# Kernel optimization log

Hardware: AMD Instinct MI355X
Metric: run time of the kernel (lower is better)

The kernel has to match this reference:

```python
import jax, jax.numpy as jnp
import numpy as np

B, L, D_IN, D_MODEL, H = 8, 1024, 256, 512, 8
D_HEAD = D_MODEL // H


def setup_inputs() -> dict:
    key = jax.random.key(0)
    ks = jax.random.split(key, 12)
    queries = jax.random.normal(ks[0], (B, L, D_IN), dtype=jnp.float32)
    keys_ = jax.random.normal(ks[1], (B, L, D_IN), dtype=jnp.float32)
    values = jax.random.normal(ks[2], (B, L, D_IN), dtype=jnp.float32)
    attention_mask = jnp.ones((B, L), dtype=jnp.int32)
    # binary symmetric-ish adjacency (sparse molecular graph style)
    adjacency_matrix = (jax.random.uniform(ks[3], (B, L, L)) < 0.05).astype(jnp.float32)
    distance_matrix = jax.random.uniform(ks[4], (B, L, L), dtype=jnp.float32) * 10.0
    s = 1.0 / np.sqrt(D_IN)
    W_q = jax.random.normal(ks[5], (D_MODEL, D_IN), dtype=jnp.float32) * s
    W_k = jax.random.normal(ks[6], (D_MODEL, D_IN), dtype=jnp.float32) * s
    W_v = jax.random.normal(ks[7], (D_MODEL, D_IN), dtype=jnp.float32) * s
    W_o = jax.random.normal(ks[8], (D_MODEL, D_MODEL), dtype=jnp.float32) / np.sqrt(D_MODEL)
    lambda_a = jax.random.normal(ks[9], (H,), dtype=jnp.float32) * 0.1
    lambda_d = jax.random.normal(ks[10], (H,), dtype=jnp.float32) * 0.1
    return {"queries": queries, "keys": keys_, "values": values,
            "attention_mask": attention_mask, "adjacency_matrix": adjacency_matrix,
            "distance_matrix": distance_matrix, "W_q": W_q, "W_k": W_k,
            "W_v": W_v, "W_o": W_o, "lambda_a": lambda_a, "lambda_d": lambda_d}


def _split_heads(x):
    # (b, l, d_model) -> (b, h, l, d_head)
    b, l, _ = x.shape
    return x.reshape(b, l, H, D_HEAD).transpose(0, 2, 1, 3)


def reference(queries, keys, values, attention_mask, adjacency_matrix,
              distance_matrix, W_q, W_k, W_v, W_o, lambda_a, lambda_d):
    Q = _split_heads(queries @ W_q.T)   # (b,h,l,d)
    K = _split_heads(keys @ W_k.T)
    V = _split_heads(values @ W_v.T)
    scores = jnp.einsum("bhqd,bhkd->bhqk", Q, K) / jnp.sqrt(jnp.asarray(D_HEAD, Q.dtype))
    # MSRSA: per-head learned scalars inject graph structure into the scores
    scores = (scores
              + lambda_a[None, :, None, None] * adjacency_matrix[:, None, :, :]
              + lambda_d[None, :, None, None] * distance_matrix[:, None, :, :])
    mask = attention_mask[:, None, None, :] > 0  # (b,1,1,l) key mask
    scores = jnp.where(mask, scores, jnp.asarray(-1e9, scores.dtype))
    attn_weight = jax.nn.softmax(scores, axis=-1)  # (b,h,l,l)
    out = jnp.einsum("bhqk,bhkd->bhqd", attn_weight, V)
    out = out.transpose(0, 2, 1, 3).reshape(queries.shape[0], queries.shape[1], D_MODEL)
    return out @ W_o.T
```

## Files before the change

### kernel.cpp

```cpp
#include <hip/hip_runtime.h>
#include <hip/hip_fp16.h>

#define BB 8
#define LL 1024
#define DIN 256
#define DM 512
#define HH 8
#define DH 64

typedef __attribute__((ext_vector_type(8))) short bf16x8;
typedef __attribute__((ext_vector_type(4))) float f32x4;

__device__ __forceinline__ unsigned short f2bf(float f) {
  union { float f; unsigned u; } c; c.f = f;
  unsigned u = c.u;
  return (unsigned short)((u + 0x7fffu + ((u >> 16) & 1u)) >> 16);
}

#if defined(__has_builtin)
#if __has_builtin(__builtin_amdgcn_cvt_pk_bf16_f32)
#define HAS_PK_BF16 1
#endif
#endif

#if defined(HAS_PK_BF16)
typedef __bf16 bf2 __attribute__((ext_vector_type(2)));
__device__ __forceinline__ unsigned pk2(float lo, float hi) {
  union { bf2 v; unsigned u; } c;
  c.v = __builtin_amdgcn_cvt_pk_bf16_f32(lo, hi);
  return c.u;
}
#else
__device__ __forceinline__ unsigned pk2(float lo, float hi) {
  return ((unsigned)f2bf(hi) << 16) | f2bf(lo);
}
#endif

__device__ __forceinline__ unsigned pk16(float a, float d) {
  unsigned v = (unsigned)__half_as_ushort(__float2half_rn(d));
  v = (v + 1u) & 0xFFFEu;
  return v | (a > 0.5f ? 1u : 0u);
}
__device__ __forceinline__ unsigned pk16x2(float a0, float d0,
                                           float a1, float d1) {
  return pk16(a0, d0) | (pk16(a1, d1) << 16);
}

__device__ __forceinline__ void async_copy16(void* lds, const void* g) {
  __builtin_amdgcn_global_load_lds(
      (const __attribute__((address_space(1))) unsigned*)g,
      (__attribute__((address_space(3))) unsigned*)lds, 16, 0, 0);
}

__global__ __launch_bounds__(256) void prep(
    const float* __restrict__ qin, const float* __restrict__ kin,
    const float* __restrict__ vin,
    const float* __restrict__ wq, const float* __restrict__ wk,
    const float* __restrict__ wv, const float* __restrict__ wo,
    const int* __restrict__ msk,
    const float* __restrict__ adj, const float* __restrict__ dis,
    unsigned short* __restrict__ xq, unsigned short* __restrict__ xk,
    unsigned short* __restrict__ xv,
    unsigned short* __restrict__ wqb, unsigned short* __restrict__ wkb,
    unsigned short* __restrict__ wvb, unsigned short* __restrict__ wob,
    float* __restrict__ mad, unsigned short* __restrict__ bp)
{
  int t = blockIdx.x * 256 + threadIdx.x;
  const int XS = 524288, WS = 32768;
  if (t < 3 * XS) {
    int seg = t >> 19, off = t & (XS - 1);
    const float* s = (seg == 0) ? qin : (seg == 1) ? kin : vin;
    unsigned short* d = (seg == 0) ? xq : (seg == 1) ? xk : xv;
    float4 f = ((const float4*)s)[off];
    uint2 o = { pk2(f.x, f.y), pk2(f.z, f.w) };
    ((uint2*)d)[off] = o;
    return;
  }
  t -= 3 * XS;
  if (t < 3 * WS) {
    int seg = t >> 15, off = t & (WS - 1);
    const float* s = (seg == 0) ? wq : (seg == 1) ? wk : wv;
    unsigned short* d = (seg == 0) ? wqb : (seg == 1) ? wkb : wvb;
    float4 f = ((const float4*)s)[off];
    uint2 o = { pk2(f.x, f.y), pk2(f.z, f.w) };
    ((uint2*)d)[off] = o;
    return;
  }
  t -= 3 * WS;
  if (t < 65536) {
    float4 f = ((const float4*)wo)[t];
    uint2 o = { pk2(f.x, f.y), pk2(f.z, f.w) };
    ((uint2*)wob)[t] = o;
    return;
  }
  t -= 65536;
  if (t < 2048) {
    int4 m = ((const int4*)msk)[t];
    float4 f = { m.x ? 0.0f : -30000.0f, m.y ? 0.0f : -30000.0f,
                 m.z ? 0.0f : -30000.0f, m.w ? 0.0f : -30000.0f };
    ((float4*)mad)[t] = f;
    return;
  }
  t -= 2048;
  if (t < 1048576) {
    float4 a0 = ((const float4*)adj)[t * 2];
    float4 a1 = ((const float4*)adj)[t * 2 + 1];
    float4 d0 = ((const float4*)dis)[t * 2];
    float4 d1 = ((const float4*)dis)[t * 2 + 1];
    uint4 o = { pk16x2(a0.x, d0.x, a0.y, d0.y),
                pk16x2(a0.z, d0.z, a0.w, d0.w),
                pk16x2(a1.x, d1.x, a1.y, d1.y),
                pk16x2(a1.z, d1.z, a1.w, d1.w) };
    ((uint4*)bp)[t] = o;
  }
}

__global__ __launch_bounds__(256) void qkv_proj(
    const unsigned short* __restrict__ xq, const unsigned short* __restrict__ xk,
    const unsigned short* __restrict__ xv,
    const unsigned short* __restrict__ wqb, const unsigned short* __restrict__ wkb,
    const unsigned short* __restrict__ wvb,
    unsigned short* __restrict__ qb, unsigned short* __restrict__ kb,
    unsigned short* __restrict__ vt)
{
  const int t = blockIdx.z;
  const unsigned short* __restrict__ X = (t == 0) ? xq : (t == 1) ? xk : xv;
  const unsigned short* __restrict__ W = (t == 0) ? wqb : (t == 1) ? wkb : wvb;
  const int m0 = blockIdx.y * 128;
  const int h  = blockIdx.x;
  __shared__ __align__(16) char arena[49152];
  const int tid = threadIdx.x;
  const int wid = tid >> 6;
  const int lane = tid & 63;
  const int lo = lane & 15;
  const int quad = lane >> 4;
  char* xpriv = arena + 32768 + wid * 4096;

  f32x4 acc[2][4];
#pragma unroll
  for (int mi = 0; mi < 2; ++mi)
#pragma unroll
    for (int ni = 0; ni < 4; ++ni) acc[mi][ni] = (f32x4)0.0f;

#pragma unroll
  for (int j = 0; j < 8; ++j) {
    int idx = j * 256 + tid, r = idx >> 5, c = idx & 31;
    async_copy16(arena + j * 4096 + wid * 1024,
                 W + (size_t)(h * 64 + r) * DIN + ((c ^ (r & 15)) * 8));
  }
#pragma unroll
  for (int j = 0; j < 2; ++j) {
    int idx = j * 64 + lane, r = idx >> 2, c = idx & 3;
    async_copy16(xpriv + j * 1024,
                 X + (size_t)(m0 + wid * 32 + r) * DIN + ((c ^ (r & 3)) * 8));
  }
  __syncthreads();

  const unsigned short* Wb = (const unsigned short*)arena;
  for (int it = 0; it < 8; ++it) {
    const int p = it & 1;
    if (it < 7) {
      const int kk = (it + 1) * 32;
#pragma unroll
      for (int j = 0; j < 2; ++j) {
        int idx = j * 64 + lane, r = idx >> 2, c = idx & 3;
        async_copy16(xpriv + (1 - p) * 2048 + j * 1024,
                     X + (size_t)(m0 + wid * 32 + r) * DIN + kk +
                         ((c ^ (r & 3)) * 8));
      }
      asm volatile("" ::: "memory");
      asm volatile("s_waitcnt vmcnt(2)" ::: "memory");
    } else {
      asm volatile("s_waitcnt vmcnt(0)" ::: "memory");
    }
    const unsigned short* Ab = (const unsigned short*)(xpriv + p * 2048);
    bf16x8 a[2], bfr[4];
#pragma unroll
    for (int mi = 0; mi < 2; ++mi) {
      int R = mi * 16 + lo;
      a[mi] = *(const bf16x8*)&Ab[R * 32 + ((quad ^ (R & 3)) * 8)];
    }
#pragma unroll
    for (int ni = 0; ni < 4; ++ni) {
      int N = ni * 16 + lo;
      bfr[ni] = *(const bf16x8*)&Wb[N * 256 + (((it * 4 + quad) ^ (N & 15)) * 8)];
    }
#pragma unroll
    for (int mi = 0; mi < 2; ++mi)
#pragma unroll
      for (int ni = 0; ni < 4; ++ni)
        acc[mi][ni] = __builtin_amdgcn_mfma_f32_16x16x32_bf16(
            a[mi], bfr[ni], acc[mi][ni], 0, 0, 0);
  }

  const int b = m0 >> 10;
  const int lbase0 = (m0 & 1023) + wid * 32;
  if (t < 2) {
    unsigned short* dstp = (t == 0) ? qb : kb;
#pragma unroll
    for (int mi = 0; mi < 2; ++mi)
#pragma unroll
      for (int ni = 0; ni < 4; ++ni) {
        int d = ni * 16 + lo;
#pragma unroll
        for (int r = 0; r < 4; ++r) {
          int lb = lbase0 + mi * 16 + quad * 4 + r;
          dstp[((size_t)(b * HH + h) * LL + lb) * DH + d] = f2bf(acc[mi][ni][r]);
        }
      }
  } else {
#pragma unroll
    for (int mi = 0; mi < 2; ++mi)
#pragma unroll
      for (int ni = 0; ni < 4; ++ni) {
        int d = ni * 16 + lo;
        int lb = lbase0 + quad * 8 + mi * 4;
        uint2 o = { pk2(acc[mi][ni][0], acc[mi][ni][1]),
                    pk2(acc[mi][ni][2], acc[mi][ni][3]) };
        *(uint2*)&vt[((size_t)(b * HH + h) * DH + d) * LL + lb] = o;
      }
  }
}

__global__ __launch_bounds__(256) void attn(
    const unsigned short* __restrict__ qb, const unsigned short* __restrict__ kb,
    const unsigned short* __restrict__ vt,
    const float* __restrict__ mad, const unsigned short* __restrict__ bp,
    const float* __restrict__ la_, const float* __restrict__ ld_,
    unsigned short* __restrict__ ao)
{
  const int bi = blockIdx.x;
  const int b  = bi & 7;
  const int hg = (bi >> 3) & 3;
  const int q0 = (bi >> 5) * 32;
  const int tid = threadIdx.x;
  const int wid = tid >> 6;
  const int lane = tid & 63;
  const int lo = lane & 15;
  const int quad = lane >> 4;
  const int h  = hg * 2 + (wid & 1);
  const int kh = wid >> 1;
  const int bh = b * HH + h;

  __shared__ __align__(16) char arena[40960];
  float* mgbuf = (float*)arena;

  const float LOG2E = 1.44269504f;
  const float la2 = la_[h] * LOG2E, ld2 = ld_[h] * LOG2E;
  const float sc2 = 0.125f * LOG2E;

  const unsigned short* qp = qb + ((size_t)bh * LL + q0) * DH;
  bf16x8 qB[2][2];
#pragma unroll
  for (int nj = 0; nj < 2; ++nj)
#pragma unroll
    for (int ki = 0; ki < 2; ++ki)
      qB[nj][ki] = *(const bf16x8*)&qp[(nj * 16 + lo) * DH + ki * 32 + quad * 8];

  const unsigned short* kp = kb + (size_t)bh * LL * DH;
  const unsigned short* vp = vt + (size_t)bh * DH * LL;
  const unsigned short* bpp = bp + ((size_t)b * LL + q0) * LL;
  const float* mp = mad + b * LL;

  f32x4 o[4][2];
  float rs[2] = {0.0f, 0.0f};
#pragma unroll
  for (int md = 0; md < 4; ++md)
#pragma unroll
    for (int nj = 0; nj < 2; ++nj) o[md][nj] = (f32x4)0.0f;

  const int kbeg = kh * (LL / 2);
  const int r8 = lane >> 3, p8 = lane & 7;
  const int br = lane >> 2;
  const int bsw = ((((lane & 3) << 1) ^ (br & 6)) << 2);

  {
    const unsigned short* kg = kp + (size_t)kbeg * DH;
#pragma unroll
    for (int j = 0; j < 4; ++j)
      async_copy16(arena + wid * 4096 + j * 1024,
                   kg + (j * 8 + r8) * 64 + ((p8 ^ r8) * 8));
    if ((wid & 1) == 0) {
      const int khs = wid >> 1;
      const unsigned short* bg = bpp + khs * (LL / 2);
#pragma unroll
      for (int j = 0; j < 2; ++j)
        async_copy16(arena + 32768 + khs * 2048 + j * 1024,
                     bg + (size_t)(j * 16 + br) * LL + bsw);
    }
  }
  __syncthreads();

  for (int jt = 0; jt < 16; ++jt) {
    const int p = jt & 1;
    const int k0 = kbeg + jt * 32;

    if (jt < 15) {
      const int kn = k0 + 32, q = 1 - p;
      const unsigned short* kg = kp + (size_t)kn * DH;
#pragma unroll
      for (int j = 0; j < 4; ++j)
        async_copy16(arena + q * 16384 + wid * 4096 + j * 1024,
                     kg + (j * 8 + r8) * 64 + ((p8 ^ r8) * 8));
      if ((wid & 1) == 0) {
        const int khs = wid >> 1;
        const unsigned short* bg = bpp + khs * (LL / 2) + (jt + 1) * 32;
#pragma unroll
        for (int j = 0; j < 2; ++j)
          async_copy16(arena + 32768 + q * 4096 + khs * 2048 + j * 1024,
                       bg + (size_t)(j * 16 + br) * LL + bsw);
      }
    }

    bf16x8 vA[4];
#pragma unroll
    for (int md = 0; md < 4; ++md)
      vA[md] = *(const bf16x8*)&vp[(md * 16 + lo) * LL + k0 + quad * 8];
    f32x4 msv[2];
#pragma unroll
    for (int mi = 0; mi < 2; ++mi)
      msv[mi] = *(const f32x4*)&mp[k0 + mi * 16 + quad * 4];

    asm volatile("" ::: "memory");

    const unsigned short* kbf = (const unsigned short*)(arena + p * 16384) + wid * 2048;
    bf16x8 kA[2][2];
#pragma unroll
    for (int mi = 0; mi < 2; ++mi)
#pragma unroll
      for (int ki = 0; ki < 2; ++ki)
        kA[mi][ki] = *(const bf16x8*)&kbf[(mi * 16 + lo) * 64 +
                                          (((ki * 4 + quad) ^ (lo & 7)) * 8)];
    f32x4 s[2][2];
#pragma unroll
    for (int mi = 0; mi < 2; ++mi)
#pragma unroll
      for (int nj = 0; nj < 2; ++nj) s[mi][nj] = (f32x4)0.0f;
#pragma unroll
    for (int ki = 0; ki < 2; ++ki)
#pragma unroll
      for (int mi = 0; mi < 2; ++mi)
#pragma unroll
        for (int nj = 0; nj < 2; ++nj)
          s[mi][nj] = __builtin_amdgcn_mfma_f32_16x16x32_bf16(
              kA[mi][ki], qB[nj][ki], s[mi][nj], 0, 0, 0);

    const unsigned short* bbf =
        (const unsigned short*)(arena + 32768 + p * 4096) + kh * 1024;
    unsigned pw[2][4];
#pragma unroll
    for (int mi = 0; mi < 2; ++mi)
#pragma unroll
      for (int nj = 0; nj < 2; ++nj) {
        uint2 w = *(const uint2*)&bbf[(nj * 16 + lo) * 32 +
                                      (((mi * 4 + quad) ^ (lo & 6)) << 2)];
        float p4[4];
#pragma unroll
        for (int r = 0; r < 4; ++r) {
          unsigned xr = (((r & 2) ? w.y : w.x) >> ((r & 1) * 16)) & 0xFFFFu;
          float dv = __half2float(__ushort_as_half(
              (unsigned short)(xr & 0xFFFEu)));
          float tb = fmaf(s[mi][nj][r], sc2, msv[mi][r]);
          tb = fmaf(dv, ld2, tb);
          tb += (xr & 1u) ? la2 : 0.0f;
          p4[r] = __builtin_amdgcn_exp2f(tb);
        }
        rs[nj] += (p4[0] + p4[1]) + (p4[2] + p4[3]);
        pw[nj][mi * 2]     = pk2(p4[0], p4[1]);
        pw[nj][mi * 2 + 1] = pk2(p4[2], p4[3]);
      }
    bf16x8 pB[2];
#pragma unroll
    for (int nj = 0; nj < 2; ++nj) {
      union { unsigned u[4]; bf16x8 v; } pc;
      pc.u[0] = pw[nj][0]; pc.u[1] = pw[nj][1];
      pc.u[2] = pw[nj][2]; pc.u[3] = pw[nj][3];
      pB[nj] = pc.v;
    }

#pragma unroll
    for (int md = 0; md < 4; ++md)
#pragma unroll
      for (int nj = 0; nj < 2; ++nj)
        o[md][nj] = __builtin_amdgcn_mfma_f32_16x16x32_bf16(
            vA[md], pB[nj], o[md][nj], 0, 0, 0);

    __syncthreads();
  }

  const int hs = wid & 1;
  if (kh == 1) {
#pragma unroll
    for (int md = 0; md < 4; ++md)
#pragma unroll
      for (int nj = 0; nj < 2; ++nj)
#pragma unroll
        for (int r = 0; r < 4; ++r)
          mgbuf[hs * 2176 + ((md * 2 + nj) * 4 + r) * 64 + lane] = o[md][nj][r];
    mgbuf[hs * 2176 + 32 * 64 + lane] = rs[0];
    mgbuf[hs * 2176 + 33 * 64 + lane] = rs[1];
  }
  __syncthreads();
  if (kh == 0) {
#pragma unroll
    for (int md = 0; md < 4; ++md)
#pragma unroll
      for (int nj = 0; nj < 2; ++nj)
#pragma unroll
        for (int r = 0; r < 4; ++r)
          o[md][nj][r] += mgbuf[hs * 2176 + ((md * 2 + nj) * 4 + r) * 64 + lane];
    rs[0] += mgbuf[hs * 2176 + 32 * 64 + lane];
    rs[1] += mgbuf[hs * 2176 + 33 * 64 + lane];
    float inv[2];
#pragma unroll
    for (int nj = 0; nj < 2; ++nj) {
      rs[nj] += __shfl_xor(rs[nj], 16);
      rs[nj] += __shfl_xor(rs[nj], 32);
      inv[nj] = __builtin_amdgcn_rcpf(rs[nj]);
    }
#pragma unroll
    for (int md = 0; md < 4; ++md)
#pragma unroll
      for (int nj = 0; nj < 2; ++nj) {
        int l = q0 + nj * 16 + lo;
        uint2 st = { pk2(o[md][nj][0] * inv[nj], o[md][nj][1] * inv[nj]),
                     pk2(o[md][nj][2] * inv[nj], o[md][nj][3] * inv[nj]) };
        *(uint2*)&ao[((size_t)b * LL + l) * DM + h * DH + md * 16 + quad * 4] = st;
      }
  }
}

__global__ __launch_bounds__(256) void oproj(
    const unsigned short* __restrict__ ao, const unsigned short* __restrict__ wob,
    float* __restrict__ out)
{
  const int m0 = blockIdx.y * 128;
  const int n0 = blockIdx.x * 64;
  __shared__ __align__(16) char arena[81920];
  const int tid = threadIdx.x;
  const int wid = tid >> 6;
  const int lane = tid & 63;
  const int lo = lane & 15;
  const int quad = lane >> 4;
  char* xpriv = arena + 65536 + wid * 4096;

  f32x4 acc[2][4];
#pragma unroll
  for (int mi = 0; mi < 2; ++mi)
#pragma unroll
    for (int ni = 0; ni < 4; ++ni) acc[mi][ni] = (f32x4)0.0f;

#pragma unroll
  for (int j = 0; j < 16; ++j) {
    int idx = j * 256 + tid, r = idx >> 6, c = idx & 63;
    async_copy16(arena + j * 4096 + wid * 1024,
                 wob + (size_t)(n0 + r) * DM + ((c ^ (r & 15)) * 8));
  }
#pragma unroll
  for (int j = 0; j < 2; ++j) {
    int idx = j * 64 + lane, r = idx >> 2, c = idx & 3;
    async_copy16(xpriv + j * 1024,
                 ao + (size_t)(m0 + wid * 32 + r) * DM + ((c ^ (r & 3)) * 8));
  }
  __syncthreads();

  const unsigned short* Wb = (const unsigned short*)arena;
  for (int it = 0; it < 16; ++it) {
    const int p = it & 1;
    if (it < 15) {
      const int kk = (it + 1) * 32;
#pragma unroll
      for (int j = 0; j < 2; ++j) {
        int idx = j * 64 + lane, r = idx >> 2, c = idx & 3;
        async_copy16(xpriv + (1 - p) * 2048 + j * 1024,
                     ao + (size_t)(m0 + wid * 32 + r) * DM + kk +
                         ((c ^ (r & 3)) * 8));
      }
      asm volatile("" ::: "memory");
      asm volatile("s_waitcnt vmcnt(2)" ::: "memory");
    } else {
      asm volatile("s_waitcnt vmcnt(0)" ::: "memory");
    }
    const unsigned short* Ab = (const unsigned short*)(xpriv + p * 2048);
    bf16x8 a[2], bfr[4];
#pragma unroll
    for (int mi = 0; mi < 2; ++mi) {
      int R = mi * 16 + lo;
      a[mi] = *(const bf16x8*)&Ab[R * 32 + ((quad ^ (R & 3)) * 8)];
    }
#pragma unroll
    for (int ni = 0; ni < 4; ++ni) {
      int N = ni * 16 + lo;
      bfr[ni] = *(const bf16x8*)&Wb[N * 512 + (((it * 4 + quad) ^ (N & 15)) * 8)];
    }
#pragma unroll
    for (int mi = 0; mi < 2; ++mi)
#pragma unroll
      for (int ni = 0; ni < 4; ++ni)
        acc[mi][ni] = __builtin_amdgcn_mfma_f32_16x16x32_bf16(
            a[mi], bfr[ni], acc[mi][ni], 0, 0, 0);
  }

#pragma unroll
  for (int mi = 0; mi < 2; ++mi)
#pragma unroll
    for (int ni = 0; ni < 4; ++ni)
#pragma unroll
      for (int r = 0; r < 4; ++r)
        out[(size_t)(m0 + wid * 32 + mi * 16 + quad * 4 + r) * DM +
            n0 + ni * 16 + lo] = acc[mi][ni][r];
}

extern "C" void kernel_launch(void* const* d_in, const int* in_sizes, int n_in,
                              void* d_out, int out_size, void* d_ws, size_t ws_size,
                              hipStream_t stream) {
  const float* qin = (const float*)d_in[0];
  const float* kin = (const float*)d_in[1];
  const float* vin = (const float*)d_in[2];
  const int*   msk = (const int*)d_in[3];
  const float* adj = (const float*)d_in[4];
  const float* dis = (const float*)d_in[5];
  const float* wq  = (const float*)d_in[6];
  const float* wk  = (const float*)d_in[7];
  const float* wv  = (const float*)d_in[8];
  const float* wo  = (const float*)d_in[9];
  const float* la  = (const float*)d_in[10];
  const float* ld  = (const float*)d_in[11];
  float* out = (float*)d_out;

  const size_t tensb = (size_t)BB * HH * LL * DH;
  const size_t xsz   = (size_t)BB * LL * DIN;
  unsigned short* qb  = (unsigned short*)d_ws;
  unsigned short* kb  = qb + tensb;
  unsigned short* vt  = kb + tensb;
  unsigned short* ao  = vt + tensb;
  unsigned short* xq  = ao;
  unsigned short* xk  = ao + xsz;
  unsigned short* xv  = ao + tensb;
  unsigned short* wqb = xv + xsz;
  unsigned short* wkb = wqb + (size_t)DM * DIN;
  unsigned short* wvb = wkb + (size_t)DM * DIN;
  unsigned short* wob = wvb + (size_t)DM * DIN;
  float*          mdd = (float*)(wob + (size_t)DM * DM);
  unsigned short* bpk = (unsigned short*)(mdd + (size_t)BB * LL);

  prep<<<dim3(10888), 256, 0, stream>>>(qin, kin, vin, wq, wk, wv, wo, msk,
                                        adj, dis,
                                        xq, xk, xv, wqb, wkb, wvb, wob, mdd, bpk);
  qkv_proj<<<dim3(8, 64, 3), 256, 0, stream>>>(xq, xk, xv, wqb, wkb, wvb, qb, kb, vt);
  attn<<<dim3(1024), 256, 0, stream>>>(qb, kb, vt, mdd, bpk, la, ld, ao);
  oproj<<<dim3(8, 64), 256, 0, stream>>>(ao, wob, out);
}
```

Baseline: 230.7 us.

## Use per-wave private LDS buffers and drop per-iteration block barriers

Each wave now owns its own K tile (single-buffered) and its own double-buffered copy of the bias tile in LDS, so the per-iteration __syncthreads is replaced by explicit vmcnt/lgkmcnt waits. The next K tile is prefetched into the same buffer right after its LDS reads complete, and the bias tile is now loaded redundantly by both head waves instead of being shared. This removes block-wide barrier stalls and cuts LDS use, which may allow more blocks per CU, at the cost of duplicated bias loads and reliance on hand-counted vmcnt values that must match the compiler's memory-op ordering.

New measurement: 226.3 us, median of 2. About the same (-1.9%).

```diff
diff --git a/kernel.cpp b/kernel.cpp
--- a/kernel.cpp
+++ b/kernel.cpp
@@ -242,7 +242,9 @@
   const int kh = wid >> 1;
   const int bh = b * HH + h;
 
-  __shared__ __align__(16) char arena[40960];
+  __shared__ __align__(16) char arena[32768];
+  char* kpriv = arena + wid * 4096;
+  char* bpriv = arena + 16384 + wid * 4096;
   float* mgbuf = (float*)arena;
 
   const float LOG2E = 1.44269504f;
@@ -275,41 +277,26 @@
   const int bsw = ((((lane & 3) << 1) ^ (br & 6)) << 2);
 
   {
+    const unsigned short* bg = bpp + kh * (LL / 2);
+#pragma unroll
+    for (int j = 0; j < 2; ++j)
+      async_copy16(bpriv + j * 1024, bg + (size_t)(j * 16 + br) * LL + bsw);
     const unsigned short* kg = kp + (size_t)kbeg * DH;
 #pragma unroll
     for (int j = 0; j < 4; ++j)
-      async_copy16(arena + wid * 4096 + j * 1024,
-                   kg + (j * 8 + r8) * 64 + ((p8 ^ r8) * 8));
-    if ((wid & 1) == 0) {
-      const int khs = wid >> 1;
-      const unsigned short* bg = bpp + khs * (LL / 2);
-#pragma unroll
-      for (int j = 0; j < 2; ++j)
-        async_copy16(arena + 32768 + khs * 2048 + j * 1024,
-                     bg + (size_t)(j * 16 + br) * LL + bsw);
-    }
-  }
-  __syncthreads();
+      async_copy16(kpriv + j * 1024, kg + (j * 8 + r8) * 64 + ((p8 ^ r8) * 8));
+  }
 
   for (int jt = 0; jt < 16; ++jt) {
     const int p = jt & 1;
     const int k0 = kbeg + jt * 32;
 
     if (jt < 15) {
-      const int kn = k0 + 32, q = 1 - p;
-      const unsigned short* kg = kp + (size_t)kn * DH;
-#pragma unroll
-      for (int j = 0; j < 4; ++j)
-        async_copy16(arena + q * 16384 + wid * 4096 + j * 1024,
-                     kg + (j * 8 + r8) * 64 + ((p8 ^ r8) * 8));
-      if ((wid & 1) == 0) {
-        const int khs = wid >> 1;
-        const unsigned short* bg = bpp + khs * (LL / 2) + (jt + 1) * 32;
-#pragma unroll
-        for (int j = 0; j < 2; ++j)
-          async_copy16(arena + 32768 + q * 4096 + khs * 2048 + j * 1024,
-                       bg + (size_t)(j * 16 + br) * LL + bsw);
-      }
+      const unsigned short* bg = bpp + kh * (LL / 2) + (jt + 1) * 32;
+#pragma unroll
+      for (int j = 0; j < 2; ++j)
+        async_copy16(bpriv + (1 - p) * 2048 + j * 1024,
+                     bg + (size_t)(j * 16 + br) * LL + bsw);
     }
 
     bf16x8 vA[4];
@@ -320,17 +307,40 @@
 #pragma unroll
     for (int mi = 0; mi < 2; ++mi)
       msv[mi] = *(const f32x4*)&mp[k0 + mi * 16 + quad * 4];
-
     asm volatile("" ::: "memory");
 
-    const unsigned short* kbf = (const unsigned short*)(arena + p * 16384) + wid * 2048;
+    if (jt < 15) {
+      asm volatile("s_waitcnt vmcnt(7)" ::: "memory");
+    } else {
+      asm volatile("s_waitcnt vmcnt(5)" ::: "memory");
+    }
+
     bf16x8 kA[2][2];
 #pragma unroll
     for (int mi = 0; mi < 2; ++mi)
 #pragma unroll
       for (int ki = 0; ki < 2; ++ki)
-        kA[mi][ki] = *(const bf16x8*)&kbf[(mi * 16 + lo) * 64 +
-                                          (((ki * 4 + quad) ^ (lo & 7)) * 8)];
+        kA[mi][ki] = *(const bf16x8*)&((const unsigned short*)kpriv)
+            [(mi * 16 + lo) * 64 + (((ki * 4 + quad) ^ (lo & 7)) * 8)];
+    const unsigned short* bbf = (const unsigned short*)(bpriv + p * 2048);
+    uint2 w[2][2];
+#pragma unroll
+    for (int mi = 0; mi < 2; ++mi)
+#pragma unroll
+      for (int nj = 0; nj < 2; ++nj)
+        w[mi][nj] = *(const uint2*)&bbf[(nj * 16 + lo) * 32 +
+                                        (((mi * 4 + quad) ^ (lo & 6)) << 2)];
+
+    asm volatile("s_waitcnt lgkmcnt(0)" ::: "memory");
+    if (jt < 15) {
+      const unsigned short* kg = kp + (size_t)(k0 + 32) * DH;
+#pragma unroll
+      for (int j = 0; j < 4; ++j)
+        async_copy16(kpriv + j * 1024,
+                     kg + (j * 8 + r8) * 64 + ((p8 ^ r8) * 8));
+    }
+    asm volatile("" ::: "memory");
+
     f32x4 s[2][2];
 #pragma unroll
     for (int mi = 0; mi < 2; ++mi)
@@ -345,19 +355,16 @@
           s[mi][nj] = __builtin_amdgcn_mfma_f32_16x16x32_bf16(
               kA[mi][ki], qB[nj][ki], s[mi][nj], 0, 0, 0);
 
-    const unsigned short* bbf =
-        (const unsigned short*)(arena + 32768 + p * 4096) + kh * 1024;
     unsigned pw[2][4];
 #pragma unroll
     for (int mi = 0; mi < 2; ++mi)
 #pragma unroll
       for (int nj = 0; nj < 2; ++nj) {
-        uint2 w = *(const uint2*)&bbf[(nj * 16 + lo) * 32 +
-                                      (((mi * 4 + quad) ^ (lo & 6)) << 2)];
         float p4[4];
 #pragma unroll
         for (int r = 0; r < 4; ++r) {
-          unsigned xr = (((r & 2) ? w.y : w.x) >> ((r & 1) * 16)) & 0xFFFFu;
+          unsigned xr = (((r & 2) ? w[mi][nj].y : w[mi][nj].x) >>
+                         ((r & 1) * 16)) & 0xFFFFu;
           float dv = __half2float(__ushort_as_half(
               (unsigned short)(xr & 0xFFFEu)));
           float tb = fmaf(s[mi][nj][r], sc2, msv[mi][r]);
@@ -384,10 +391,9 @@
       for (int nj = 0; nj < 2; ++nj)
         o[md][nj] = __builtin_amdgcn_mfma_f32_16x16x32_bf16(
             vA[md], pB[nj], o[md][nj], 0, 0, 0);
-
-    __syncthreads();
-  }
-
+  }
+
+  __syncthreads();
   const int hs = wid & 1;
   if (kh == 1) {
 #pragma unroll
```
